# Performance work log

Hardware: AMD Instinct MI355X
Metric: run time of the kernel (lower is better)

## Reference

```python
import jax, jax.numpy as jnp
import numpy as np


def _conv1x1(x, W, b):
    # 1x1 conv == per-pixel channel matmul: x [B,C,H,W], W [O,C], b [O]
    return jnp.einsum('bchw,oc->bohw', x, W) + b[None, :, None, None]


def setup_inputs() -> dict:
    key = jax.random.key(0)
    ks = jax.random.split(key, 9)
    B, C, H, W = 16, 512, 32, 32
    s = 1.0 / np.sqrt(C)
    inp = {
        'x': jax.random.normal(ks[0], (B, C, H, W), dtype=jnp.float32),
        'Wq': jax.random.normal(ks[1], (C, C), dtype=jnp.float32) * s,
        'bq': jax.random.normal(ks[2], (C,), dtype=jnp.float32) * 0.01,
        'Wk': jax.random.normal(ks[3], (C, C), dtype=jnp.float32) * s,
        'bk': jax.random.normal(ks[4], (C,), dtype=jnp.float32) * 0.01,
        'Wv': jax.random.normal(ks[5], (C, C), dtype=jnp.float32) * s,
        'bv': jax.random.normal(ks[6], (C,), dtype=jnp.float32) * 0.01,
        'Wo': jax.random.normal(ks[7], (C, C), dtype=jnp.float32) * s,
        'bo': jax.random.normal(ks[8], (C,), dtype=jnp.float32) * 0.01,
    }
    return inp


def reference(x, Wq, bq, Wk, bk, Wv, bv, Wo, bo):
    B, C, H, W = x.shape
    q = _conv1x1(x, Wq, bq)
    k = _conv1x1(x, Wk, bk)
    v = _conv1x1(x, Wv, bv)
    hw = H * W
    qf = q.reshape(B, C, hw)  # [B,C,HW]
    kf = k.reshape(B, C, hw)
    vf = v.reshape(B, C, hw)
    # scores[b,i,j] = sum_c q[b,c,i] * k[b,c,j], scaled by c^-0.5
    scores = jnp.einsum('bci,bcj->bij', qf, kf) * (C ** -0.5)
    attn = jax.nn.softmax(scores, axis=2)  # softmax over keys j
    # out[b,c,i] = sum_j v[b,c,j] * attn[b,i,j]
    out = jnp.einsum('bcj,bij->bci', vf, attn).reshape(B, C, H, W)
    out = _conv1x1(out, Wo, bo)
    return x + out
```

## Files before the change

### kernel.cpp

```cpp
#include <hip/hip_runtime.h>
#include <hip/hip_bf16.h>
#include <math.h>


typedef __bf16 bf16x8 __attribute__((ext_vector_type(8)));
typedef float  f32x4  __attribute__((ext_vector_type(4)));

__device__ __forceinline__ unsigned short f2bf(float f) {
    unsigned u = __float_as_uint(f);
    u += 0x7fff + ((u >> 16) & 1);
    return (unsigned short)(u >> 16);
}

__device__ __forceinline__ float bf2f(unsigned short h) {
    return __uint_as_float(((unsigned)h) << 16);
}

__device__ __forceinline__ void gload_lds16(const void* g, void* l) {
    __builtin_amdgcn_global_load_lds(
        (const __attribute__((address_space(1))) void*)g,
        (__attribute__((address_space(3))) void*)l, 16, 0, 0);
}

__device__ __forceinline__ void decode_tile(int L, int ln_nn, int ln_pb,
                                            int& bz, int& m0, int& n0) {
    const int xcd = L & 7;
    const int idx = L >> 3;
    bz = xcd * 2 + (idx >> ln_pb);
    const int w = idx & ((1 << ln_pb) - 1);
    m0 = (w >> ln_nn) << 7;
    n0 = (w & ((1 << ln_nn) - 1)) << 7;
}

__device__ __forceinline__ void mfma_kloop(
    const unsigned short* __restrict__ A, const unsigned short* __restrict__ B,
    int K, int ldA, int ldB, int m0, int n0,
    unsigned short* als, unsigned short* bls,
    f32x4 (&acc)[4][4])
{
    const int tid  = threadIdx.x;
    const int lane = tid & 63;
    const int wave = tid >> 6;
    const int wm   = wave >> 1;
    const int wn   = wave & 1;

    const int ar = lane >> 2;
    const int ak = (lane & 3) * 8;

    const unsigned short* agp = A + (long)(m0 + wave * 16 + ar) * ldA + ak;
    const unsigned short* bgp = B + (long)(n0 + wave * 16 + ar) * ldB + ak;
    const long aj = 64L * ldA;
    const long bj = 64L * ldB;
    unsigned short* al0  = als + wave * 512;
    unsigned short* al0h = als + (wave + 4) * 512;
    unsigned short* al1  = als + 4096 + wave * 512;
    unsigned short* al1h = als + 4096 + (wave + 4) * 512;
    unsigned short* bl0  = bls + wave * 512;
    unsigned short* bl0h = bls + (wave + 4) * 512;
    unsigned short* bl1  = bls + 4096 + wave * 512;
    unsigned short* bl1h = bls + 4096 + (wave + 4) * 512;

    const int fr = lane & 15;
    const int fq = lane >> 4;

    for (int k0 = 0; k0 < K; k0 += 64) {
        gload_lds16(agp,           al0);
        gload_lds16(agp + aj,      al0h);
        gload_lds16(agp + 32,      al1);
        gload_lds16(agp + 32 + aj, al1h);
        gload_lds16(bgp,           bl0);
        gload_lds16(bgp + bj,      bl0h);
        gload_lds16(bgp + 32,      bl1);
        gload_lds16(bgp + 32 + bj, bl1h);
        agp += 64; bgp += 64;
        __syncthreads();

        #pragma unroll
        for (int p = 0; p < 2; ++p) {
            bf16x8 af[4], bfr[4];
            #pragma unroll
            for (int mt = 0; mt < 4; ++mt)
                af[mt] = *(const bf16x8*)&als[p * 4096 + (wm * 64 + mt * 16 + fr) * 32 + fq * 8];
            #pragma unroll
            for (int nt = 0; nt < 4; ++nt)
                bfr[nt] = *(const bf16x8*)&bls[p * 4096 + (wn * 64 + nt * 16 + fr) * 32 + fq * 8];

            #pragma unroll
            for (int mt = 0; mt < 4; ++mt)
                #pragma unroll
                for (int nt = 0; nt < 4; ++nt)
                    acc[mt][nt] = __builtin_amdgcn_mfma_f32_16x16x32_bf16(
                        af[mt], bfr[nt], acc[mt][nt], 0, 0, 0);
        }
        __syncthreads();
    }
}

__global__ __launch_bounds__(256) void gemm_plain2(
    const unsigned short* __restrict__ A0, const unsigned short* __restrict__ B0,
    unsigned short* __restrict__ C0, const float* __restrict__ bias0,
    int N0, int K0, int ldA0, int ldB0, long sA0, long sB0, long sC0,
    int ln_nn0, int ln_pb0, int nb0,
    const unsigned short* __restrict__ A1, const unsigned short* __restrict__ B1,
    unsigned short* __restrict__ C1, const float* __restrict__ bias1,
    int N1, int K1, int ldA1, int ldB1, long sA1, long sB1, long sC1,
    int ln_nn1, int ln_pb1)
{
    __shared__ unsigned short Als[2 * 128 * 32];
    __shared__ unsigned short Bls[2 * 128 * 32];

    int L = blockIdx.x;
    const unsigned short *A, *B;
    unsigned short* C;
    const float* bias;
    int N, K, ldA, ldB, ln_nn, ln_pb;
    long sA, sB, sC;
    if (L < nb0) {
        A = A0; B = B0; C = C0; bias = bias0;
        N = N0; K = K0; ldA = ldA0; ldB = ldB0;
        sA = sA0; sB = sB0; sC = sC0; ln_nn = ln_nn0; ln_pb = ln_pb0;
    } else {
        L -= nb0;
        A = A1; B = B1; C = C1; bias = bias1;
        N = N1; K = K1; ldA = ldA1; ldB = ldB1;
        sA = sA1; sB = sB1; sC = sC1; ln_nn = ln_nn1; ln_pb = ln_pb1;
    }

    int bz, m0, n0;
    decode_tile(L, ln_nn, ln_pb, bz, m0, n0);

    f32x4 acc[4][4] = {};
    mfma_kloop(A + bz * sA, B + bz * sB, K, ldA, ldB, m0, n0, Als, Bls, acc);

    const int lane = threadIdx.x & 63;
    const int wave = threadIdx.x >> 6;
    const int wm = wave >> 1, wn = wave & 1;
    const int fr = lane & 15, fq = lane >> 4;

    unsigned short* Ch = C + bz * sC;
    #pragma unroll
    for (int nt = 0; nt < 4; ++nt) {
        const int col = n0 + wn * 64 + nt * 16 + fr;
        const float bn = bias ? bias[col] : 0.0f;
        #pragma unroll
        for (int mt = 0; mt < 4; ++mt) {
            const int row = m0 + wm * 64 + mt * 16 + fq * 4;
            #pragma unroll
            for (int r = 0; r < 4; ++r)
                Ch[(long)(row + r) * N + col] = f2bf(acc[mt][nt][r] + bn);
        }
    }
}

__global__ __launch_bounds__(256) void gemm_exp(
    const unsigned short* __restrict__ A, const unsigned short* __restrict__ B,
    unsigned short* __restrict__ Cout, float* __restrict__ lsum,
    int N, int K, int ldA, int ldB, long sA, long sB, long sC, long sL,
    int ln_nn, int ln_pb)
{
    __shared__ unsigned short Als[2 * 128 * 32];
    __shared__ unsigned short Bls[2 * 128 * 32];

    int bz, m0, n0;
    decode_tile(blockIdx.x, ln_nn, ln_pb, bz, m0, n0);

    f32x4 acc[4][4] = {};
    mfma_kloop(A + bz * sA, B + bz * sB, K, ldA, ldB, m0, n0, Als, Bls, acc);

    const int lane = threadIdx.x & 63;
    const int wave = threadIdx.x >> 6;
    const int wm = wave >> 1, wn = wave & 1;
    const int fr = lane & 15, fq = lane >> 4;

    unsigned short* Ch = Cout + bz * sC;
    float* lrow = lsum + bz * sL;
    #pragma unroll
    for (int mt = 0; mt < 4; ++mt) {
        const int row = m0 + wm * 64 + mt * 16 + fq * 4;
        #pragma unroll
        for (int r = 0; r < 4; ++r) {
            float rs = 0.0f;
            #pragma unroll
            for (int nt = 0; nt < 4; ++nt) {
                const int col = n0 + wn * 64 + nt * 16 + fr;
                const float e = __expf(acc[mt][nt][r]);
                rs += e;
                Ch[(long)(row + r) * N + col] = f2bf(e);
            }
            rs += __shfl_xor(rs, 1);
            rs += __shfl_xor(rs, 2);
            rs += __shfl_xor(rs, 4);
            rs += __shfl_xor(rs, 8);
            if (fr == 0) atomicAdd(&lrow[row + r], rs);
        }
    }
}

__global__ __launch_bounds__(256) void gemm_final(
    const unsigned short* __restrict__ A, const unsigned short* __restrict__ B,
    float* __restrict__ Cout, const float* __restrict__ biasM,
    const unsigned short* __restrict__ resid, const float* __restrict__ lsum,
    int N, int K, int ldA, int ldB, long sA, long sB, long sC, long sR, long sL,
    int ln_nn, int ln_pb)
{
    __shared__ unsigned short Als[2 * 128 * 32];
    __shared__ unsigned short Bls[2 * 128 * 32];

    int bz, m0, n0;
    decode_tile(blockIdx.x, ln_nn, ln_pb, bz, m0, n0);

    f32x4 acc[4][4] = {};
    mfma_kloop(A + bz * sA, B + bz * sB, K, ldA, ldB, m0, n0, Als, Bls, acc);

    const int lane = threadIdx.x & 63;
    const int wave = threadIdx.x >> 6;
    const int wm = wave >> 1, wn = wave & 1;
    const int fr = lane & 15, fq = lane >> 4;

    float* Cf = Cout + bz * sC;
    const unsigned short* rz = resid + bz * sR;
    const float* lrow = lsum + bz * sL;
    #pragma unroll
    for (int nt = 0; nt < 4; ++nt) {
        const int col = n0 + wn * 64 + nt * 16 + fr;
        const float linv = 1.0f / lrow[col];
        #pragma unroll
        for (int mt = 0; mt < 4; ++mt) {
            const int row = m0 + wm * 64 + mt * 16 + fq * 4;
            #pragma unroll
            for (int r = 0; r < 4; ++r) {
                const long idx = (long)(row + r) * N + col;
                Cf[idx] = acc[mt][nt][r] * linv + biasM[row + r] + bf2f(rz[idx]);
            }
        }
    }
}

__global__ __launch_bounds__(256) void prep_all(
    const float* __restrict__ x,
    unsigned short* __restrict__ xT, unsigned short* __restrict__ xbf,
    const float* __restrict__ Wq, const float* __restrict__ Wk,
    const float* __restrict__ Wv, const float* __restrict__ Wo,
    const float* __restrict__ bq, const float* __restrict__ bk,
    const float* __restrict__ bv, const float* __restrict__ bo,
    unsigned short* __restrict__ Wqb, unsigned short* __restrict__ Wkb,
    unsigned short* __restrict__ Wvob,
    float* __restrict__ biasqk, float* __restrict__ bvo,
    float* __restrict__ lsum)
{
    const float s = 0.044194173824159216f;
    const int b = blockIdx.x;
    const int t = threadIdx.x;

    if (b < 256) {
        __shared__ float Ao[32][33];
        __shared__ float Bv[32][33];
        const int m0 = (b >> 4) * 32;
        const int n0 = (b & 15) * 32;
        const int tx = t & 31;
        const int ty = t >> 5;
        float acc[4] = {0.f, 0.f, 0.f, 0.f};
        for (int k0 = 0; k0 < 512; k0 += 32) {
            #pragma unroll
            for (int i = 0; i < 4; ++i)
                Ao[ty + 8 * i][tx] = Wo[(long)(m0 + ty + 8 * i) * 512 + k0 + tx];
            #pragma unroll
            for (int i = 0; i < 4; ++i)
                Bv[ty + 8 * i][tx] = Wv[(long)(k0 + ty + 8 * i) * 512 + n0 + tx];
            __syncthreads();
            #pragma unroll
            for (int kk = 0; kk < 32; ++kk) {
                const float bvv = Bv[kk][tx];
                #pragma unroll
                for (int i = 0; i < 4; ++i)
                    acc[i] += Ao[ty * 4 + i][kk] * bvv;
            }
            __syncthreads();
        }
        #pragma unroll
        for (int i = 0; i < 4; ++i)
            Wvob[(long)(m0 + ty * 4 + i) * 512 + n0 + tx] = f2bf(acc[i]);
    } else if (b < 264) {
        const int o = (b - 256) * 64 + (t >> 2);
        const int q = t & 3;
        const float4* wrow = (const float4*)(Wo + (long)o * 512 + q * 128);
        const float4* bvv4 = (const float4*)(bv + q * 128);
        float p = 0.f;
        #pragma unroll
        for (int i = 0; i < 32; ++i) {
            const float4 w = wrow[i];
            const float4 v = bvv4[i];
            p += w.x * v.x + w.y * v.y + w.z * v.z + w.w * v.w;
        }
        __shared__ float red[256];
        red[t] = p;
        __syncthreads();
        if (q == 0) bvo[o] = red[t] + red[t + 1] + red[t + 2] + red[t + 3] + bo[o];
    } else if (b == 264) {
        biasqk[t]       = bq[t] * s;
        biasqk[256 + t] = bq[256 + t] * s;
        biasqk[512 + t] = bk[t];
        biasqk[768 + t] = bk[256 + t];
        #pragma unroll
        for (int i = 0; i < 64; ++i) lsum[i * 256 + t] = 0.0f;
    } else if (b < 777) {
        const bool isq = b < 521;
        const float* src = isq ? Wq : Wk;
        unsigned short* dst = isq ? Wqb : Wkb;
        const float m = isq ? s : 1.0f;
        const int i = (((b - 265) & 255) * 256 + t) * 4;
        const float4 f = *(const float4*)(src + i);
        ushort4 h;
        h.x = f2bf(f.x * m); h.y = f2bf(f.y * m);
        h.z = f2bf(f.z * m); h.w = f2bf(f.w * m);
        *(ushort4*)(dst + i) = h;
    } else {
        __shared__ float tl[32][33];
        const int xb = b - 777;
        const int batch = xb >> 9;
        const int rem = xb & 511;
        const int p0 = (rem & 31) * 32;
        const int c0 = (rem >> 5) * 32;
        const float* xp = x + (long)batch * 524288;
        unsigned short* xTb  = xT  + (long)batch * 524288;
        unsigned short* xbfb = xbf + (long)batch * 524288;
        const int tx = t & 31;
        const int ty = t >> 5;
        #pragma unroll
        for (int i = 0; i < 4; ++i) {
            const float v = xp[(long)(c0 + ty + 8 * i) * 1024 + p0 + tx];
            xbfb[(long)(c0 + ty + 8 * i) * 1024 + p0 + tx] = f2bf(v);
            tl[ty + 8 * i][tx] = v;
        }
        __syncthreads();
        #pragma unroll
        for (int i = 0; i < 4; ++i)
            xTb[(long)(p0 + ty + 8 * i) * 512 + c0 + tx] = f2bf(tl[tx][ty + 8 * i]);
    }
}

extern "C" void kernel_launch(void* const* d_in, const int* in_sizes, int n_in,
                              void* d_out, int out_size, void* d_ws, size_t ws_size,
                              hipStream_t stream)
{
    const float* x  = (const float*)d_in[0];
    const float* Wq = (const float*)d_in[1];
    const float* bq = (const float*)d_in[2];
    const float* Wk = (const float*)d_in[3];
    const float* bk = (const float*)d_in[4];
    const float* Wv = (const float*)d_in[5];
    const float* bv = (const float*)d_in[6];
    const float* Wo = (const float*)d_in[7];
    const float* bo = (const float*)d_in[8];
    float* out = (float*)d_out;

    const int Bn = 16, C = 512, HW = 1024;
    const long CHW = (long)C * HW;
    const long SHW = (long)HW * HW;

    unsigned short* xT   = (unsigned short*)d_ws;
    unsigned short* qkT  = xT + Bn * CHW;
    unsigned short* xbf  = qkT + Bn * SHW;
    unsigned short* expS = xbf + Bn * CHW;
    unsigned short* Yb   = expS + Bn * SHW;
    unsigned short* Wqb  = Yb + Bn * CHW;
    unsigned short* Wkb  = Wqb + 262144;
    unsigned short* Wvob = Wkb + 262144;
    float* biasqk = (float*)(Wvob + 262144);
    float* bvo    = biasqk + 1024;
    float* lsum   = bvo + 512;

    const dim3 blk(256);

    prep_all<<<dim3(8969), blk, 0, stream>>>(
        x, xT, xbf, Wq, Wk, Wv, Wo, bq, bk, bv, bo,
        Wqb, Wkb, Wvob, biasqk, bvo, lsum);

    gemm_plain2<<<dim3(1536), blk, 0, stream>>>(
        xT, Wqb, qkT, biasqk, 2 * C, C, C, C, CHW, 0, SHW, 3, 6, 1024,
        Wvob, xT, Yb, nullptr, HW, C, C, C, 0, CHW, CHW, 3, 5);

    gemm_exp<<<dim3(1024), blk, 0, stream>>>(
        qkT, qkT + C, expS, lsum,
        HW, C, 2 * C, 2 * C, SHW, SHW, SHW, HW, 3, 6);

    gemm_final<<<dim3(512), blk, 0, stream>>>(
        Yb, expS, out, bvo, xbf, lsum,
        HW, HW, HW, HW, CHW, SHW, CHW, CHW, HW, 3, 5);
}
```

Baseline: 220.4 us.

## Fold Wq and Wk into a single Gram matrix to halve projection GEMM

Precomputes G = scale·Wqᵀ·Wk in the prep kernel and computes Zᵀ = xᵀ·G so scores become xᵀ·Z, replacing separate Q and K projections. Query-bias contributions become a per-key vector u added before exp, and key-bias terms are dropped since they are constant per softmax row. This removes half the projection GEMM work and the qkT buffer traffic, at the cost of an extra small fp32 GEMM in prep, a u reduction pass, and different bf16 rounding of the fused weight.

```diff
diff --git a/kernel.cpp b/kernel.cpp
--- a/kernel.cpp
+++ b/kernel.cpp
@@ -96,66 +96,75 @@
     }
 }
 
-__global__ __launch_bounds__(256) void gemm_plain2(
-    const unsigned short* __restrict__ A0, const unsigned short* __restrict__ B0,
-    unsigned short* __restrict__ C0, const float* __restrict__ bias0,
-    int N0, int K0, int ldA0, int ldB0, long sA0, long sB0, long sC0,
-    int ln_nn0, int ln_pb0, int nb0,
-    const unsigned short* __restrict__ A1, const unsigned short* __restrict__ B1,
-    unsigned short* __restrict__ C1, const float* __restrict__ bias1,
-    int N1, int K1, int ldA1, int ldB1, long sA1, long sB1, long sC1,
-    int ln_nn1, int ln_pb1)
+__global__ __launch_bounds__(256) void dual_zt_y_u(
+    const unsigned short* __restrict__ xT, const unsigned short* __restrict__ Gb,
+    unsigned short* __restrict__ ZTb,
+    const unsigned short* __restrict__ Wvob, unsigned short* __restrict__ Yb,
+    const float* __restrict__ g, float* __restrict__ u)
 {
     __shared__ unsigned short Als[2 * 128 * 32];
     __shared__ unsigned short Bls[2 * 128 * 32];
 
-    int L = blockIdx.x;
-    const unsigned short *A, *B;
-    unsigned short* C;
-    const float* bias;
-    int N, K, ldA, ldB, ln_nn, ln_pb;
-    long sA, sB, sC;
-    if (L < nb0) {
-        A = A0; B = B0; C = C0; bias = bias0;
-        N = N0; K = K0; ldA = ldA0; ldB = ldB0;
-        sA = sA0; sB = sB0; sC = sC0; ln_nn = ln_nn0; ln_pb = ln_pb0;
-    } else {
-        L -= nb0;
-        A = A1; B = B1; C = C1; bias = bias1;
-        N = N1; K = K1; ldA = ldA1; ldB = ldB1;
-        sA = sA1; sB = sB1; sC = sC1; ln_nn = ln_nn1; ln_pb = ln_pb1;
-    }
-
+    const long CHW = 524288;
+    const int Lb = blockIdx.x;
+
+    if (Lb >= 1024) {
+        float* gs = (float*)Als;
+        const int t = threadIdx.x;
+        gs[t] = g[t];
+        gs[t + 256] = g[t + 256];
+        __syncthreads();
+        const int idx = Lb - 1024;
+        const int batch = idx >> 2;
+        const int j = (idx & 3) * 256 + t;
+        const unsigned short* xr = xT + batch * CHW + (long)j * 512;
+        float sum = 0.0f;
+        for (int k = 0; k < 512; k += 8) {
+            const bf16x8 v = *(const bf16x8*)(xr + k);
+            #pragma unroll
+            for (int e = 0; e < 8; ++e) sum += (float)v[e] * gs[k + e];
+        }
+        u[batch * 1024 + j] = sum;
+        return;
+    }
+
+    const bool isZT = (Lb < 512);
+    const int L = isZT ? Lb : (Lb - 512);
     int bz, m0, n0;
-    decode_tile(L, ln_nn, ln_pb, bz, m0, n0);
+    if (isZT) decode_tile(L, 2, 5, bz, m0, n0);
+    else      decode_tile(L, 3, 5, bz, m0, n0);
+
+    const unsigned short* A = isZT ? (xT + bz * CHW)  : Wvob;
+    const unsigned short* B = isZT ? Gb               : (xT + bz * CHW);
+    unsigned short* Ch      = isZT ? (ZTb + bz * CHW) : (Yb + bz * CHW);
+    const int N = isZT ? 512 : 1024;
 
     f32x4 acc[4][4] = {};
-    mfma_kloop(A + bz * sA, B + bz * sB, K, ldA, ldB, m0, n0, Als, Bls, acc);
+    mfma_kloop(A, B, 512, 512, 512, m0, n0, Als, Bls, acc);
 
     const int lane = threadIdx.x & 63;
     const int wave = threadIdx.x >> 6;
     const int wm = wave >> 1, wn = wave & 1;
     const int fr = lane & 15, fq = lane >> 4;
 
-    unsigned short* Ch = C + bz * sC;
     #pragma unroll
     for (int nt = 0; nt < 4; ++nt) {
         const int col = n0 + wn * 64 + nt * 16 + fr;
-        const float bn = bias ? bias[col] : 0.0f;
         #pragma unroll
         for (int mt = 0; mt < 4; ++mt) {
             const int row = m0 + wm * 64 + mt * 16 + fq * 4;
             #pragma unroll
             for (int r = 0; r < 4; ++r)
-                Ch[(long)(row + r) * N + col] = f2bf(acc[mt][nt][r] + bn);
+                Ch[(long)(row + r) * N + col] = f2bf(acc[mt][nt][r]);
         }
     }
 }
 
 __global__ __launch_bounds__(256) void gemm_exp(
     const unsigned short* __restrict__ A, const unsigned short* __restrict__ B,
-    unsigned short* __restrict__ Cout, float* __restrict__ lsum,
-    int N, int K, int ldA, int ldB, long sA, long sB, long sC, long sL,
+    unsigned short* __restrict__ Cout, const float* __restrict__ ub,
+    float* __restrict__ lsum,
+    int N, int K, int ldA, int ldB, long sA, long sB, long sC, long sU, long sL,
     int ln_nn, int ln_pb)
 {
     __shared__ unsigned short Als[2 * 128 * 32];
@@ -171,6 +180,12 @@
     const int wave = threadIdx.x >> 6;
     const int wm = wave >> 1, wn = wave & 1;
     const int fr = lane & 15, fq = lane >> 4;
+
+    const float* ucol = ub + bz * sU;
+    float u4[4];
+    #pragma unroll
+    for (int nt = 0; nt < 4; ++nt)
+        u4[nt] = ucol[n0 + wn * 64 + nt * 16 + fr];
 
     unsigned short* Ch = Cout + bz * sC;
     float* lrow = lsum + bz * sL;
@@ -183,7 +198,7 @@
             #pragma unroll
             for (int nt = 0; nt < 4; ++nt) {
                 const int col = n0 + wn * 64 + nt * 16 + fr;
-                const float e = __expf(acc[mt][nt][r]);
+                const float e = __expf(acc[mt][nt][r] + u4[nt]);
                 rs += e;
                 Ch[(long)(row + r) * N + col] = f2bf(e);
             }
@@ -241,11 +256,10 @@
     unsigned short* __restrict__ xT, unsigned short* __restrict__ xbf,
     const float* __restrict__ Wq, const float* __restrict__ Wk,
     const float* __restrict__ Wv, const float* __restrict__ Wo,
-    const float* __restrict__ bq, const float* __restrict__ bk,
-    const float* __restrict__ bv, const float* __restrict__ bo,
-    unsigned short* __restrict__ Wqb, unsigned short* __restrict__ Wkb,
-    unsigned short* __restrict__ Wvob,
-    float* __restrict__ biasqk, float* __restrict__ bvo,
+    const float* __restrict__ bq, const float* __restrict__ bv,
+    const float* __restrict__ bo,
+    unsigned short* __restrict__ Gb, unsigned short* __restrict__ Wvob,
+    float* __restrict__ bvo, float* __restrict__ g,
     float* __restrict__ lsum)
 {
     const float s = 0.044194173824159216f;
@@ -280,8 +294,37 @@
         #pragma unroll
         for (int i = 0; i < 4; ++i)
             Wvob[(long)(m0 + ty * 4 + i) * 512 + n0 + tx] = f2bf(acc[i]);
-    } else if (b < 264) {
-        const int o = (b - 256) * 64 + (t >> 2);
+    } else if (b < 512) {
+        __shared__ float Aq[32][33];
+        __shared__ float Bk[32][33];
+        const int wb = b - 256;
+        const int c0 = (wb >> 4) * 32;
+        const int k0t = (wb & 15) * 32;
+        const int tx = t & 31;
+        const int ty = t >> 5;
+        float acc[4] = {0.f, 0.f, 0.f, 0.f};
+        for (int m0 = 0; m0 < 512; m0 += 32) {
+            #pragma unroll
+            for (int i = 0; i < 4; ++i)
+                Aq[ty + 8 * i][tx] = Wq[(long)(m0 + ty + 8 * i) * 512 + c0 + tx];
+            #pragma unroll
+            for (int i = 0; i < 4; ++i)
+                Bk[ty + 8 * i][tx] = Wk[(long)(m0 + ty + 8 * i) * 512 + k0t + tx];
+            __syncthreads();
+            #pragma unroll
+            for (int mm = 0; mm < 32; ++mm) {
+                const float bb = Bk[mm][tx];
+                #pragma unroll
+                for (int i = 0; i < 4; ++i)
+                    acc[i] += Aq[mm][ty * 4 + i] * bb;
+            }
+            __syncthreads();
+        }
+        #pragma unroll
+        for (int i = 0; i < 4; ++i)
+            Gb[(long)(c0 + ty * 4 + i) * 512 + k0t + tx] = f2bf(s * acc[i]);
+    } else if (b < 520) {
+        const int o = (b - 512) * 64 + (t >> 2);
         const int q = t & 3;
         const float4* wrow = (const float4*)(Wo + (long)o * 512 + q * 128);
         const float4* bvv4 = (const float4*)(bv + q * 128);
@@ -296,27 +339,24 @@
         red[t] = p;
         __syncthreads();
         if (q == 0) bvo[o] = red[t] + red[t + 1] + red[t + 2] + red[t + 3] + bo[o];
-    } else if (b == 264) {
-        biasqk[t]       = bq[t] * s;
-        biasqk[256 + t] = bq[256 + t] * s;
-        biasqk[512 + t] = bk[t];
-        biasqk[768 + t] = bk[256 + t];
+    } else if (b < 528) {
+        const int c0 = (b - 520) * 64;
+        const int cl = t & 63;
+        const int q = t >> 6;
+        float p = 0.f;
+        for (int m = q * 128; m < q * 128 + 128; ++m)
+            p += Wk[(long)m * 512 + c0 + cl] * bq[m];
+        __shared__ float red[256];
+        red[t] = p;
+        __syncthreads();
+        if (q == 0)
+            g[c0 + cl] = s * (red[cl] + red[cl + 64] + red[cl + 128] + red[cl + 192]);
+    } else if (b == 528) {
         #pragma unroll
         for (int i = 0; i < 64; ++i) lsum[i * 256 + t] = 0.0f;
-    } else if (b < 777) {
-        const bool isq = b < 521;
-        const float* src = isq ? Wq : Wk;
-        unsigned short* dst = isq ? Wqb : Wkb;
-        const float m = isq ? s : 1.0f;
-        const int i = (((b - 265) & 255) * 256 + t) * 4;
-        const float4 f = *(const float4*)(src + i);
-        ushort4 h;
-        h.x = f2bf(f.x * m); h.y = f2bf(f.y * m);
-        h.z = f2bf(f.z * m); h.w = f2bf(f.w * m);
-        *(ushort4*)(dst + i) = h;
     } else {
         __shared__ float tl[32][33];
-        const int xb = b - 777;
+        const int xb = b - 529;
         const int batch = xb >> 9;
         const int rem = xb & 511;
         const int p0 = (rem & 31) * 32;
@@ -347,7 +387,6 @@
     const float* Wq = (const float*)d_in[1];
     const float* bq = (const float*)d_in[2];
     const float* Wk = (const float*)d_in[3];
-    const float* bk = (const float*)d_in[4];
     const float* Wv = (const float*)d_in[5];
     const float* bv = (const float*)d_in[6];
     const float* Wo = (const float*)d_in[7];
@@ -359,30 +398,28 @@
     const long SHW = (long)HW * HW;
 
     unsigned short* xT   = (unsigned short*)d_ws;
-    unsigned short* qkT  = xT + Bn * CHW;
-    unsigned short* xbf  = qkT + Bn * SHW;
+    unsigned short* xbf  = xT + Bn * CHW;
     unsigned short* expS = xbf + Bn * CHW;
-    unsigned short* Yb   = expS + Bn * SHW;
-    unsigned short* Wqb  = Yb + Bn * CHW;
-    unsigned short* Wkb  = Wqb + 262144;
-    unsigned short* Wvob = Wkb + 262144;
-    float* biasqk = (float*)(Wvob + 262144);
-    float* bvo    = biasqk + 1024;
-    float* lsum   = bvo + 512;
+    unsigned short* ZTb  = expS + Bn * SHW;
+    unsigned short* Yb   = ZTb + Bn * CHW;
+    unsigned short* Gb   = Yb + Bn * CHW;
+    unsigned short* Wvob = Gb + 262144;
+    float* bvo  = (float*)(Wvob + 262144);
+    float* g    = bvo + 512;
+    float* u    = g + 512;
+    float* lsum = u + Bn * HW;
 
     const dim3 blk(256);
 
-    prep_all<<<dim3(8969), blk, 0, stream>>>(
-        x, xT, xbf, Wq, Wk, Wv, Wo, bq, bk, bv, bo,
-        Wqb, Wkb, Wvob, biasqk, bvo, lsum);
-
-    gemm_plain2<<<dim3(1536), blk, 0, stream>>>(
-        xT, Wqb, qkT, biasqk, 2 * C, C, C, C, CHW, 0, SHW, 3, 6, 1024,
-        Wvob, xT, Yb, nullptr, HW, C, C, C, 0, CHW, CHW, 3, 5);
+    prep_all<<<dim3(8721), blk, 0, stream>>>(
+        x, xT, xbf, Wq, Wk, Wv, Wo, bq, bv, bo,
+        Gb, Wvob, bvo, g, lsum);
+
+    dual_zt_y_u<<<dim3(1088), blk, 0, stream>>>(xT, Gb, ZTb, Wvob, Yb, g, u);
 
     gemm_exp<<<dim3(1024), blk, 0, stream>>>(
-        qkT, qkT + C, expS, lsum,
-        HW, C, 2 * C, 2 * C, SHW, SHW, SHW, HW, 3, 6);
+        xT, ZTb, expS, u, lsum,
+        HW, C, C, C, CHW, CHW, SHW, HW, HW, 3, 6);
 
     gemm_final<<<dim3(512), blk, 0, stream>>>(
         Yb, expS, out, bvo, xbf, lsum,
```

New measurement: 233.1 us. 5.8% more time.
